# Performance work log

Measured on AMD Instinct MI355X. Metric: run time of the kernel, lower is better.

## Reference

```python
import jax, jax.numpy as jnp
import numpy as np

B, S, D, H = 16, 512, 1024, 16
DH = D // H  # 64


def setup_inputs() -> dict:
    key = jax.random.key(0)
    kx, kq, kk, kv = jax.random.split(key, 4)
    stdv = 1.0 / np.sqrt(DH)  # reset_param uses 1/sqrt(t.size(1)) = 1/sqrt(head_dim)
    x = jax.random.normal(kx, (B, S, D), dtype=jnp.float32)
    Wq = jax.random.uniform(kq, (H, D, DH), dtype=jnp.float32, minval=-stdv, maxval=stdv)
    Wk = jax.random.uniform(kk, (H, D, DH), dtype=jnp.float32, minval=-stdv, maxval=stdv)
    Wv = jax.random.uniform(kv, (H, D, DH), dtype=jnp.float32, minval=-stdv, maxval=stdv)
    return {"x": x, "Wq": Wq, "Wk": Wk, "Wv": Wv}


def reference(x, Wq, Wk, Wv):
    # x: [B, S, D]; Wq/Wk/Wv: [H, D, DH] (stacked per-head params)
    q = jnp.einsum('bsd,hde->bhse', x, Wq)  # [B,H,S,DH]
    k = jnp.einsum('bsd,hde->bhse', x, Wk)
    v = jnp.einsum('bsd,hde->bhse', x, Wv)
    # NOTE: original scales by sqrt(input_dim), not sqrt(head_dim)
    scale = 1.0 / jnp.sqrt(jnp.float32(D))
    scores = jnp.einsum('bhse,bhte->bhst', q, k) * scale  # [B,H,S,S]
    attn = jax.nn.softmax(scores, axis=-1)
    out = jnp.einsum('bhst,bhte->bhse', attn, v)  # [B,H,S,DH]
    # concat heads along feature dim (head order matches torch cat over loop)
    return out.transpose(0, 2, 1, 3).reshape(x.shape[0], x.shape[1], D)
```

## Files before the change

kernel.cpp:

```cpp
#include <hip/hip_runtime.h>
#include <math.h>

constexpr int B = 16, S = 512, D = 1024, H = 16, DH = 64;
constexpr int BH = B * H;

typedef short bf16x8 __attribute__((ext_vector_type(8)));
typedef float f32x4  __attribute__((ext_vector_type(4)));

__device__ __forceinline__ unsigned short f2bf(float f) {
    unsigned u = __float_as_uint(f);
    u += 0x7fff + ((u >> 16) & 1);
    return (unsigned short)(u >> 16);
}

#define VMC0  asm volatile("s_waitcnt vmcnt(0)" ::: "memory")
#define BARR  __builtin_amdgcn_s_barrier()

__global__ __launch_bounds__(256) void convert_x(
    const float* __restrict__ x, unsigned short* __restrict__ xb)
{
    int i = blockIdx.x * 256 + threadIdx.x;
    float4 v = ((const float4*)x)[i];
    ushort4 o;
    o.x = f2bf(v.x); o.y = f2bf(v.y); o.z = f2bf(v.z); o.w = f2bf(v.w);
    ((ushort4*)xb)[i] = o;
}

__global__ __launch_bounds__(256) void convert_w(
    const float* __restrict__ Wq, const float* __restrict__ Wk,
    const float* __restrict__ Wv, unsigned short* __restrict__ WbT)
{
    __shared__ float tile[64][65];
    const int d0 = blockIdx.x * 64;
    const int h = blockIdx.y, m = blockIdx.z;
    const float* W = ((m == 0) ? Wq : (m == 1) ? Wk : Wv) + (size_t)h * D * DH;
    const int t = threadIdx.x;
    {
        int e = t & 63, dr = t >> 6;
        #pragma unroll
        for (int i = 0; i < 16; ++i) {
            int d = dr * 16 + i;
            tile[d][e] = W[(size_t)(d0 + d) * DH + e];
        }
    }
    __syncthreads();
    {
        int d = t & 63, er = t >> 6;
        unsigned short* out = WbT + (size_t)(m * H + h) * DH * D;
        #pragma unroll
        for (int i = 0; i < 16; ++i) {
            int e = er * 16 + i;
            out[(size_t)e * D + d0 + d] = f2bf(tile[d][e]);
        }
    }
}

__global__ __launch_bounds__(256) void qkv_gemm(
    const unsigned short* __restrict__ xb,
    const unsigned short* __restrict__ WbT,
    unsigned short* __restrict__ qkvb)
{
    __shared__ unsigned short As[128 * 64];
    __shared__ unsigned short Bs[128 * 64];

    const int t = threadIdx.x;
    const int w = t >> 6;
    const int wr = w >> 1, wc = w & 1;
    const int L = t & 63;
    const int lane15 = L & 15;
    const int quad = L >> 4;
    const int lrow8 = L >> 3;
    const int lg = L & 7;

    const int r0 = blockIdx.x * 128;
    const int n0 = blockIdx.y * 128;

    f32x4 acc[4][4] = {};

    for (int k0 = 0; k0 < D; k0 += 64) {
        #pragma unroll
        for (int i = 0; i < 4; ++i) {
            int c = w * 4 + i;
            int r = c * 8 + lrow8;
            int gg = lg ^ (r & 7);
            const unsigned short* gp = xb + (size_t)(r0 + r) * D + k0 + gg * 8;
            __builtin_amdgcn_global_load_lds(
                (const __attribute__((address_space(1))) void*)gp,
                (__attribute__((address_space(3))) void*)(As + c * 512),
                16, 0, 0);
            const unsigned short* gq = WbT + (size_t)(n0 + r) * D + k0 + gg * 8;
            __builtin_amdgcn_global_load_lds(
                (const __attribute__((address_space(1))) void*)gq,
                (__attribute__((address_space(3))) void*)(Bs + c * 512),
                16, 0, 0);
        }
        __syncthreads();

        #pragma unroll
        for (int ks = 0; ks < 2; ++ks) {
            int gk = ks * 4 + quad;
            bf16x8 a[4], bb[4];
            #pragma unroll
            for (int rt = 0; rt < 4; ++rt) {
                int ml = wr * 64 + rt * 16 + lane15;
                a[rt] = *(const bf16x8*)(As + ml * 64 + ((gk ^ (ml & 7)) * 8));
            }
            #pragma unroll
            for (int ct = 0; ct < 4; ++ct) {
                int nl = wc * 64 + ct * 16 + lane15;
                bb[ct] = *(const bf16x8*)(Bs + nl * 64 + ((gk ^ (nl & 7)) * 8));
            }
            #pragma unroll
            for (int rt = 0; rt < 4; ++rt)
                #pragma unroll
                for (int ct = 0; ct < 4; ++ct)
                    acc[rt][ct] = __builtin_amdgcn_mfma_f32_16x16x32_bf16(
                        a[rt], bb[ct], acc[rt][ct], 0, 0, 0);
        }
        __syncthreads();
    }

    const int m  = n0 >> 10;
    const int h  = ((n0 >> 6) + wc) & 15;
    const int bb_ = r0 >> 9;
    const int s0 = (r0 & 511) + wr * 64;

    if (m == 2) {
        unsigned short* outv = qkvb + ((size_t)(2 * BH) + (bb_ * H + h)) * (size_t)(S * DH);
        #pragma unroll
        for (int rt = 0; rt < 4; ++rt) {
            int srow = s0 + rt * 16 + quad * 4;
            #pragma unroll
            for (int ct = 0; ct < 4; ++ct) {
                int e = ct * 16 + lane15;
                ushort4 pk;
                pk.x = f2bf(acc[rt][ct][0]);
                pk.y = f2bf(acc[rt][ct][1]);
                pk.z = f2bf(acc[rt][ct][2]);
                pk.w = f2bf(acc[rt][ct][3]);
                *(ushort4*)(outv + (size_t)e * S + srow) = pk;
            }
        }
    } else {
        const float sc = (m == 0) ? 0.04508422002778011f : 1.0f;
        unsigned short* out = qkvb + ((size_t)m * BH + (bb_ * H + h)) * (size_t)(S * DH);
        #pragma unroll
        for (int rt = 0; rt < 4; ++rt) {
            #pragma unroll
            for (int ct = 0; ct < 4; ++ct) {
                int e = ct * 16 + lane15;
                #pragma unroll
                for (int r = 0; r < 4; ++r) {
                    int srow = s0 + rt * 16 + quad * 4 + r;
                    out[(size_t)srow * DH + e] = f2bf(acc[rt][ct][r] * sc);
                }
            }
        }
    }
}

__device__ __forceinline__ void stage_kv(
    const unsigned short* __restrict__ kb, const unsigned short* __restrict__ vt,
    int kt, unsigned short* Kd, unsigned short* Vd, int w, int lrow8, int lg)
{
    #pragma unroll
    for (int i = 0; i < 2; ++i) {
        int base = (w * 2 + i) * 8;
        int r = base + lrow8;
        int gr = (r & 32) | ((r & 12) << 1) | ((r & 16) >> 2) | (r & 3);
        int gg = lg ^ (r & 7);
        __builtin_amdgcn_global_load_lds(
            (const __attribute__((address_space(1))) void*)
                (kb + (size_t)(kt + gr) * DH + gg * 8),
            (__attribute__((address_space(3))) void*)(Kd + base * 64),
            16, 0, 0);
        __builtin_amdgcn_global_load_lds(
            (const __attribute__((address_space(1))) void*)
                (vt + (size_t)r * S + kt + gg * 8),
            (__attribute__((address_space(3))) void*)(Vd + base * 64),
            16, 0, 0);
    }
}

__global__ __launch_bounds__(256) void attn_mfma(
    const unsigned short* __restrict__ qkvb, float* __restrict__ out)
{
    __shared__ unsigned short Qs[128 * 64];
    __shared__ unsigned short Ks[2][64 * 64];
    __shared__ unsigned short Vt[2][64 * 64];

    const int t = threadIdx.x;
    const int w = t >> 6;
    const int L = t & 63;
    const int lane15 = L & 15;
    const int quad = L >> 4;
    const int lrow8 = L >> 3;
    const int lg = L & 7;
    const int qr0 = blockIdx.x * 128;
    const int bh = blockIdx.y;
    const int b = bh >> 4, h = bh & 15;

    const unsigned short* qb = qkvb + (size_t)bh * S * DH;
    const unsigned short* kb = qkvb + (size_t)(BH + bh) * S * DH;
    const unsigned short* vt = qkvb + (size_t)(2 * BH + bh) * S * DH;

    #pragma unroll
    for (int i = 0; i < 4; ++i) {
        int base = w * 32 + i * 8;
        int r = base + lrow8;
        int gg = lg ^ (r & 7);
        const unsigned short* gp = qb + (size_t)(qr0 + r) * DH + gg * 8;
        __builtin_amdgcn_global_load_lds(
            (const __attribute__((address_space(1))) void*)gp,
            (__attribute__((address_space(3))) void*)(Qs + base * 64),
            16, 0, 0);
    }
    stage_kv(kb, vt, 0, &Ks[0][0], &Vt[0][0], w, lrow8, lg);
    VMC0;
    BARR;

    bf16x8 qf[2][2];
    #pragma unroll
    for (int mt = 0; mt < 2; ++mt)
        #pragma unroll
        for (int ks = 0; ks < 2; ++ks) {
            int ml = w * 32 + mt * 16 + lane15;
            int gk = ks * 4 + quad;
            qf[mt][ks] = *(const bf16x8*)(Qs + ml * 64 + ((gk ^ (lane15 & 7)) * 8));
        }

    f32x4 o[2][4] = {};
    float plsum[2] = {0.f, 0.f};

    #pragma unroll 2
    for (int kt = 0; kt < S; kt += 64) {
        const int cur = (kt >> 6) & 1;
        const int nxt = cur ^ 1;

        if (kt + 64 < S)
            stage_kv(kb, vt, kt + 64, &Ks[nxt][0], &Vt[nxt][0], w, lrow8, lg);

        f32x4 st[2][4] = {};
        #pragma unroll
        for (int ks = 0; ks < 2; ++ks) {
            int gk = ks * 4 + quad;
            bf16x8 kf[4];
            #pragma unroll
            for (int ct = 0; ct < 4; ++ct) {
                int kr = ct * 16 + lane15;
                kf[ct] = *(const bf16x8*)(&Ks[cur][0] + kr * 64 + ((gk ^ (lane15 & 7)) * 8));
            }
            __builtin_amdgcn_s_setprio(1);
            #pragma unroll
            for (int mt = 0; mt < 2; ++mt)
                #pragma unroll
                for (int ct = 0; ct < 4; ++ct)
                    st[mt][ct] = __builtin_amdgcn_mfma_f32_16x16x32_bf16(
                        kf[ct], qf[mt][ks], st[mt][ct], 0, 0, 0);
            __builtin_amdgcn_s_setprio(0);
        }

        bf16x8 pB[2][2];
        #pragma unroll
        for (int mt = 0; mt < 2; ++mt) {
            float rs = 0.f;
            #pragma unroll
            for (int ct = 0; ct < 4; ++ct) {
                float p0 = exp2f(st[mt][ct][0]);
                float p1 = exp2f(st[mt][ct][1]);
                float p2 = exp2f(st[mt][ct][2]);
                float p3 = exp2f(st[mt][ct][3]);
                rs += (p0 + p1) + (p2 + p3);
                int hi = (ct & 1) * 4;
                pB[mt][ct >> 1][hi + 0] = (short)f2bf(p0);
                pB[mt][ct >> 1][hi + 1] = (short)f2bf(p1);
                pB[mt][ct >> 1][hi + 2] = (short)f2bf(p2);
                pB[mt][ct >> 1][hi + 3] = (short)f2bf(p3);
            }
            plsum[mt] += rs;
        }

        #pragma unroll
        for (int ks = 0; ks < 2; ++ks) {
            int gk = ks * 4 + quad;
            bf16x8 vf[4];
            #pragma unroll
            for (int nt = 0; nt < 4; ++nt) {
                int dh = nt * 16 + lane15;
                vf[nt] = *(const bf16x8*)(&Vt[cur][0] + dh * 64 + ((gk ^ (lane15 & 7)) * 8));
            }
            __builtin_amdgcn_s_setprio(1);
            #pragma unroll
            for (int mt = 0; mt < 2; ++mt)
                #pragma unroll
                for (int nt = 0; nt < 4; ++nt)
                    o[mt][nt] = __builtin_amdgcn_mfma_f32_16x16x32_bf16(
                        vf[nt], pB[mt][ks], o[mt][nt], 0, 0, 0);
            __builtin_amdgcn_s_setprio(0);
        }

        VMC0;
        BARR;
    }

    #pragma unroll
    for (int mt = 0; mt < 2; ++mt) {
        float l = plsum[mt];
        l += __shfl_xor(l, 16, 64);
        l += __shfl_xor(l, 32, 64);
        float inv = 1.0f / l;
        int srow = qr0 + w * 32 + mt * 16 + lane15;
        float* op = out + (size_t)(b * S + srow) * D + h * DH;
        #pragma unroll
        for (int nt = 0; nt < 4; ++nt) {
            float4 v;
            v.x = o[mt][nt][0] * inv;
            v.y = o[mt][nt][1] * inv;
            v.z = o[mt][nt][2] * inv;
            v.w = o[mt][nt][3] * inv;
            *(float4*)(op + nt * 16 + quad * 4) = v;
        }
    }
}

extern "C" void kernel_launch(void* const* d_in, const int* in_sizes, int n_in,
                              void* d_out, int out_size, void* d_ws, size_t ws_size,
                              hipStream_t stream) {
    const float* x  = (const float*)d_in[0];
    const float* Wq = (const float*)d_in[1];
    const float* Wk = (const float*)d_in[2];
    const float* Wv = (const float*)d_in[3];
    float* outp = (float*)d_out;

    unsigned short* qkvb = (unsigned short*)d_ws;
    unsigned short* xb   = (unsigned short*)((char*)d_ws + 50331648);
    unsigned short* WbT  = (unsigned short*)((char*)d_ws + 67108864);

    convert_x<<<dim3((B * S * D / 4) / 256), 256, 0, stream>>>(x, xb);
    convert_w<<<dim3(D / 64, H, 3), 256, 0, stream>>>(Wq, Wk, Wv, WbT);
    qkv_gemm<<<dim3(B * S / 128, 3 * H * DH / 128), 256, 0, stream>>>(xb, WbT, qkvb);
    attn_mfma<<<dim3(S / 128, BH), 256, 0, stream>>>(qkvb, outp);
}
```

Measured before the change: 196.8 us.

## Coalesce Q/K epilogue via LDS, hoist K/V fragment loads, use packed bf16 convert

The projection epilogue for Q and K now stages results through a swizzled LDS tile and writes 16-byte rows to global memory, replacing scattered 2-byte stores. In the attention loop, all K and V fragments for the current tile are loaded from LDS up front, before the next tile's prefetch is issued, so the MFMA chains run without interleaved LDS waits. The probability conversion uses the hardware packed v_cvt_pk_bf16_f32 instruction instead of manual rounding. Holding all K/V fragments raises register pressure, and the epilogue reuses As/Bs, which needs those buffers to be free at that point.

```diff
diff --git a/kernel.cpp b/kernel.cpp
--- a/kernel.cpp
+++ b/kernel.cpp
@@ -143,18 +143,25 @@
         }
     } else {
         const float sc = (m == 0) ? 0.04508422002778011f : 1.0f;
-        unsigned short* out = qkvb + ((size_t)m * BH + (bb_ * H + h)) * (size_t)(S * DH);
-        #pragma unroll
-        for (int rt = 0; rt < 4; ++rt) {
+        unsigned short* eb = (w < 2) ? (As + w * 4096) : (Bs + (w - 2) * 4096);
+        #pragma unroll
+        for (int rt = 0; rt < 4; ++rt)
             #pragma unroll
             for (int ct = 0; ct < 4; ++ct) {
                 int e = ct * 16 + lane15;
                 #pragma unroll
                 for (int r = 0; r < 4; ++r) {
-                    int srow = s0 + rt * 16 + quad * 4 + r;
-                    out[(size_t)srow * DH + e] = f2bf(acc[rt][ct][r] * sc);
+                    int row = rt * 16 + quad * 4 + r;
+                    eb[row * 64 + (((e >> 3) ^ (row & 7)) * 8) + (e & 7)] =
+                        f2bf(acc[rt][ct][r] * sc);
                 }
             }
+        unsigned short* outq = qkvb + ((size_t)m * BH + (bb_ * H + h)) * (size_t)(S * DH);
+        #pragma unroll
+        for (int j = 0; j < 8; ++j) {
+            int row = j * 8 + lrow8;
+            bf16x8 vv = *(const bf16x8*)(eb + row * 64 + ((lg ^ (row & 7)) * 8));
+            *(bf16x8*)(outq + (size_t)(s0 + row) * DH + lg * 8) = vv;
         }
     }
 }
@@ -237,33 +244,39 @@
         const int cur = (kt >> 6) & 1;
         const int nxt = cur ^ 1;
 
+        bf16x8 kf[2][4], vf[2][4];
+        #pragma unroll
+        for (int ks = 0; ks < 2; ++ks) {
+            int gk = ks * 4 + quad;
+            #pragma unroll
+            for (int ct = 0; ct < 4; ++ct) {
+                int kr = ct * 16 + lane15;
+                kf[ks][ct] = *(const bf16x8*)(&Ks[cur][0] + kr * 64 + ((gk ^ (lane15 & 7)) * 8));
+                vf[ks][ct] = *(const bf16x8*)(&Vt[cur][0] + kr * 64 + ((gk ^ (lane15 & 7)) * 8));
+            }
+        }
+        __builtin_amdgcn_sched_barrier(0);
+
         if (kt + 64 < S)
             stage_kv(kb, vt, kt + 64, &Ks[nxt][0], &Vt[nxt][0], w, lrow8, lg);
 
         f32x4 st[2][4] = {};
-        #pragma unroll
-        for (int ks = 0; ks < 2; ++ks) {
-            int gk = ks * 4 + quad;
-            bf16x8 kf[4];
-            #pragma unroll
-            for (int ct = 0; ct < 4; ++ct) {
-                int kr = ct * 16 + lane15;
-                kf[ct] = *(const bf16x8*)(&Ks[cur][0] + kr * 64 + ((gk ^ (lane15 & 7)) * 8));
-            }
-            __builtin_amdgcn_s_setprio(1);
+        __builtin_amdgcn_s_setprio(1);
+        #pragma unroll
+        for (int ks = 0; ks < 2; ++ks)
             #pragma unroll
             for (int mt = 0; mt < 2; ++mt)
                 #pragma unroll
                 for (int ct = 0; ct < 4; ++ct)
                     st[mt][ct] = __builtin_amdgcn_mfma_f32_16x16x32_bf16(
-                        kf[ct], qf[mt][ks], st[mt][ct], 0, 0, 0);
-            __builtin_amdgcn_s_setprio(0);
-        }
+                        kf[ks][ct], qf[mt][ks], st[mt][ct], 0, 0, 0);
+        __builtin_amdgcn_s_setprio(0);
 
         bf16x8 pB[2][2];
         #pragma unroll
         for (int mt = 0; mt < 2; ++mt) {
             float rs = 0.f;
+            union { unsigned u[4]; bf16x8 v; } pu[2];
             #pragma unroll
             for (int ct = 0; ct < 4; ++ct) {
                 float p0 = exp2f(st[mt][ct][0]);
@@ -271,33 +284,27 @@
                 float p2 = exp2f(st[mt][ct][2]);
                 float p3 = exp2f(st[mt][ct][3]);
                 rs += (p0 + p1) + (p2 + p3);
-                int hi = (ct & 1) * 4;
-                pB[mt][ct >> 1][hi + 0] = (short)f2bf(p0);
-                pB[mt][ct >> 1][hi + 1] = (short)f2bf(p1);
-                pB[mt][ct >> 1][hi + 2] = (short)f2bf(p2);
-                pB[mt][ct >> 1][hi + 3] = (short)f2bf(p3);
-            }
+                unsigned lo, hi;
+                asm("v_cvt_pk_bf16_f32 %0, %1, %2" : "=v"(lo) : "v"(p0), "v"(p1));
+                asm("v_cvt_pk_bf16_f32 %0, %1, %2" : "=v"(hi) : "v"(p2), "v"(p3));
+                pu[ct >> 1].u[(ct & 1) * 2 + 0] = lo;
+                pu[ct >> 1].u[(ct & 1) * 2 + 1] = hi;
+            }
+            pB[mt][0] = pu[0].v;
+            pB[mt][1] = pu[1].v;
             plsum[mt] += rs;
         }
 
-        #pragma unroll
-        for (int ks = 0; ks < 2; ++ks) {
-            int gk = ks * 4 + quad;
-            bf16x8 vf[4];
-            #pragma unroll
-            for (int nt = 0; nt < 4; ++nt) {
-                int dh = nt * 16 + lane15;
-                vf[nt] = *(const bf16x8*)(&Vt[cur][0] + dh * 64 + ((gk ^ (lane15 & 7)) * 8));
-            }
-            __builtin_amdgcn_s_setprio(1);
+        __builtin_amdgcn_s_setprio(1);
+        #pragma unroll
+        for (int ks = 0; ks < 2; ++ks)
             #pragma unroll
             for (int mt = 0; mt < 2; ++mt)
                 #pragma unroll
                 for (int nt = 0; nt < 4; ++nt)
                     o[mt][nt] = __builtin_amdgcn_mfma_f32_16x16x32_bf16(
-                        vf[nt], pB[mt][ks], o[mt][nt], 0, 0, 0);
-            __builtin_amdgcn_s_setprio(0);
-        }
+                        vf[ks][nt], pB[mt][ks], o[mt][nt], 0, 0, 0);
+        __builtin_amdgcn_s_setprio(0);
 
         VMC0;
         BARR;
```

Result: no change. 193.0 us (-1.9%).
